# Optimization experiments

Measured on AMD Instinct MI355X. Metric: run time of the kernel, lower is better.

The kernel has to match this reference:

```python
import jax, jax.numpy as jnp
import numpy as np

B, L, C = 4, 2048, 2048
NH, HD, K = 32, 64, 16  # num_heads, head_dim, inner chunk size
LR = 1.0
EPS = 1e-6


def ln_fwd(x, w, b):
    # F.layer_norm over last dim (biased variance), eps=1e-6
    mu = x.mean(-1, keepdims=True)
    var = x.var(-1, keepdims=True)
    xhat = (x - mu) * jax.lax.rsqrt(var + EPS)
    return w * xhat + b


def ln_fused_l2_bwd(x, target, w, b):
    # grad wrt x of 0.5*||LN(x;w,b) - target||^2 fused with LN fwd
    D = x.shape[-1]
    mu = x.mean(-1, keepdims=True)
    var = x.var(-1, keepdims=True)
    std = jnp.sqrt(var + EPS)
    xhat = (x - mu) / std
    y = w * xhat + b
    g = (y - target) * w  # dL/d(xhat)
    return (D * g - g.sum(-1, keepdims=True) - xhat * (g * xhat).sum(-1, keepdims=True)) / (D * std)


def _inner_scan(XC, XB, XA, coeff, W1, b1, lnw, lnb):
    # per (batch, head): XC/XB/XA [n_chunk,K,HD], coeff [n_chunk,K,1], W1 [HD,HD], b1 [1,HD], lnw/lnb [HD]
    mask = jnp.tril(jnp.ones((K, K), XC.dtype))

    def step(carry, inp):
        W1c, b1c = carry
        xc, xb, xa, co = inp
        Z1 = xb @ W1c + b1c                       # [K,HD]
        grad = ln_fused_l2_bwd(Z1, xa - xb, lnw, lnb)
        Attn1 = mask * (xc @ xb.T)                # [K,K] causal
        b1_bar = b1c - (co * mask) @ grad         # [K,HD]
        Z1_bar = xc @ W1c - (co * Attn1) @ grad + b1_bar
        W1n = W1c - (co[-1] * xb).T @ grad        # fast-weight update with last coeff
        b1n = b1_bar[-1:]
        out = xc + ln_fwd(Z1_bar, lnw, lnb)       # post-LN residual
        return (W1n, b1n), out

    _, ys = jax.lax.scan(step, (W1, b1), (XC, XB, XA, coeff))
    return ys.reshape(-1, HD)  # [L,HD]


def setup_inputs() -> dict:
    key = jax.random.key(0)
    ks = jax.random.split(key, 9)
    s = 0.02
    return {
        'hidden_states': jax.random.normal(ks[0], (B, L, C), jnp.float32),
        'Wq': jax.random.normal(ks[1], (C, NH * HD), jnp.float32) * s,
        'Wk': jax.random.normal(ks[2], (C, NH * HD), jnp.float32) * s,
        'Wv': jax.random.normal(ks[3], (C, NH * HD), jnp.float32) * s,
        'Wo': jax.random.normal(ks[4], (NH * HD, C), jnp.float32) * s,
        'ilr_w': jax.random.normal(ks[5], (C, NH), jnp.float32) * s,
        'ilr_b': jnp.zeros((NH,), jnp.float32),
        'ln_weight': jnp.ones((NH, HD), jnp.float32),
        'ln_bias': jnp.zeros((NH, HD), jnp.float32),
        'W1': jax.random.normal(ks[6], (NH, HD, HD), jnp.float32) * s,
        'b1': jnp.zeros((NH, 1, HD), jnp.float32),
    }


def reference(hidden_states, Wq, Wk, Wv, Wo, ilr_w, ilr_b, ln_weight, ln_bias, W1, b1):
    n_chunk = L // K

    def split(x):  # [B,L,NH*HD] -> [B,NH,n_chunk,K,HD]
        return x.reshape(B, n_chunk, K, NH, HD).transpose(0, 3, 1, 2, 4)

    XC = split(hidden_states @ Wq)
    XB = split(hidden_states @ Wk)
    XA = split(hidden_states @ Wv)

    # sigmoid-gated per-token learning rates
    ilr = jax.nn.sigmoid(hidden_states @ ilr_w + ilr_b)          # [B,L,NH]
    ilr = ilr.reshape(B, n_chunk, K, NH).transpose(0, 3, 1, 2)[..., None]  # [B,NH,n_chunk,K,1]
    token_idx = 1.0 / jnp.arange(1, K + 1, dtype=jnp.float32)
    coeff = (LR * token_idx).reshape(1, 1, 1, K, 1) * ilr / HD

    per_head = jax.vmap(_inner_scan, in_axes=(0, 0, 0, 0, 0, 0, 0, 0))
    per_batch = jax.vmap(per_head, in_axes=(0, 0, 0, 0, None, None, None, None))
    XCW = per_batch(XC, XB, XA, coeff, W1, b1, ln_weight, ln_bias)  # [B,NH,L,HD]
    XCW = XCW.transpose(0, 2, 1, 3).reshape(B, L, NH * HD)
    return XCW @ Wo
```

## Files before the change

### kernel.cpp

```cpp
#include <hip/hip_runtime.h>
#include <hip/hip_bf16.h>

typedef __attribute__((ext_vector_type(8))) short bf16x8;
typedef __attribute__((ext_vector_type(4))) short bf16x4;
typedef __attribute__((ext_vector_type(4))) float f32x4;
typedef __attribute__((ext_vector_type(8))) unsigned short u16x8;
typedef unsigned short u16;

#define AS1(p) ((__attribute__((address_space(1))) void*)(p))
#define AS3(p) ((__attribute__((address_space(3))) void*)(p))
#define GLL16(g, l) __builtin_amdgcn_global_load_lds(AS1(g), AS3(l), 16, 0, 0)

__device__ __forceinline__ u16 f2bf(float x) {
  return __builtin_bit_cast(u16, __float2bfloat16(x));
}
__device__ __forceinline__ float bf2f(u16 u) {
  return __builtin_bit_cast(float, ((unsigned)u) << 16);
}
__device__ __forceinline__ f32x4 mfma16(bf16x8 a, bf16x8 b, f32x4 c) {
  return __builtin_amdgcn_mfma_f32_16x16x32_bf16(a, b, c, 0, 0, 0);
}
__device__ __forceinline__ f32x4 mfma16k(bf16x4 a, bf16x4 b, f32x4 c) {
#if defined(__HIP_DEVICE_COMPILE__)
#if __has_builtin(__builtin_amdgcn_mfma_f32_16x16x16bf16_1k)
  return __builtin_amdgcn_mfma_f32_16x16x16bf16_1k(a, b, c, 0, 0, 0);
#else
  f32x4 d;
  asm volatile("v_mfma_f32_16x16x16_bf16 %0, %1, %2, %3"
               : "=v"(d)
               : "v"(a), "v"(b), "v"(c));
  return d;
#endif
#else
  (void)a; (void)b;
  return c;
#endif
}
#define DPPADD(x, ctrl)                                                            \
  ((x) + __builtin_bit_cast(float, __builtin_amdgcn_update_dpp(                    \
             0, __builtin_bit_cast(int, (x)), (ctrl), 0xf, 0xf, true)))
__device__ __forceinline__ float rsum16(float x) {
  x = DPPADD(x, 0x128);
  x = DPPADD(x, 0x124);
  x = DPPADD(x, 0x122);
  x = DPPADD(x, 0x121);
  return x;
}

__global__ __launch_bounds__(256) void conv_bf16(const float* __restrict__ in,
                                                 u16* __restrict__ out) {
  size_t g = (size_t)blockIdx.x * 256 + threadIdx.x;
  const float4* p = reinterpret_cast<const float4*>(in) + g * 2;
  float4 a = p[0], b = p[1];
  u16x8 r;
  r[0] = f2bf(a.x); r[1] = f2bf(a.y); r[2] = f2bf(a.z); r[3] = f2bf(a.w);
  r[4] = f2bf(b.x); r[5] = f2bf(b.y); r[6] = f2bf(b.z); r[7] = f2bf(b.w);
  *reinterpret_cast<u16x8*>(out + g * 8) = r;
}

__global__ __launch_bounds__(256) void wt_conv(const float* __restrict__ W,
                                               u16* __restrict__ Wt, int Kd, int N) {
  __shared__ float t[64][65];
  const int n0 = blockIdx.x * 64, k0 = blockIdx.y * 64;
  const int tx = threadIdx.x & 63, ty = threadIdx.x >> 6;
#pragma unroll
  for (int rr = 0; rr < 16; ++rr) {
    int r = rr * 4 + ty;
    t[r][tx] = W[(size_t)(k0 + r) * N + n0 + tx];
  }
  __syncthreads();
#pragma unroll
  for (int rr = 0; rr < 16; ++rr) {
    int r = rr * 4 + ty;
    Wt[(size_t)(n0 + r) * Kd + k0 + tx] = f2bf(t[tx][r]);
  }
}

__global__ __launch_bounds__(256) void ilr_strip(const float* __restrict__ ilr_w,
                                                 u16* __restrict__ WcatT) {
  int g = blockIdx.x * 256 + threadIdx.x;
  int p = g >> 11, k = g & 2047;
  float v = (p < 32) ? ilr_w[k * 32 + p] : 0.f;
  WcatT[(size_t)(6144 + p) * 2048 + k] = f2bf(v);
}

template <int MODE>
__global__ __launch_bounds__(512) void gemm8p(const u16* __restrict__ A,
                                              const u16* __restrict__ Bt, int M, int N, int Kd,
                                              u16* __restrict__ O0, u16* __restrict__ O1,
                                              u16* __restrict__ O2,
                                              float* __restrict__ coeffOut,
                                              const float* __restrict__ ilrb,
                                              float* __restrict__ Cout) {
  __shared__ __align__(16) u16 Asm[2][2][8192];
  __shared__ __align__(16) u16 Bsm[2][2][8192];
  const int tid = threadIdx.x;
  const int lane = tid & 63, wid = tid >> 6;
  const int wr = wid >> 2, wc = wid & 3;
  const int l15 = lane & 15, l4 = lane >> 4;
  const int wc1 = wc & 1, wch = wc >> 1;
  const int swzm = (l15 & 3) ^ (((l15 >> 2) & 1) << 2);
  const int mT = blockIdx.y << 8, nT = blockIdx.x << 8;
  const int nKt = Kd >> 6;

#define STG_A(kt_, h_)                                                              \
  do {                                                                              \
    if ((kt_) < nKt) {                                                              \
      _Pragma("unroll") for (int i_ = 0; i_ < 2; ++i_) {                            \
        const int s_ = tid + 512 * i_;                                              \
        const int r_ = s_ >> 3;                                                     \
        const int sc_ = (s_ & 7) ^ (r_ & 3) ^ (((r_ >> 2) & 1) << 2);               \
        GLL16(A + (size_t)(mT + (h_) * 128 + r_) * Kd + (kt_) * 64 + sc_ * 8,       \
              &Asm[(kt_) & 1][h_][0] + s_ * 8);                                     \
      }                                                                             \
    }                                                                               \
  } while (0)
#define STG_B(kt_, h_)                                                              \
  do {                                                                              \
    if ((kt_) < nKt) {                                                              \
      _Pragma("unroll") for (int i_ = 0; i_ < 2; ++i_) {                            \
        const int s_ = tid + 512 * i_;                                              \
        const int r_ = s_ >> 3;                                                     \
        const int sc_ = (s_ & 7) ^ (r_ & 3) ^ (((r_ >> 2) & 1) << 2);               \
        const int rg_ = nT + (h_) * 128 + r_;                                       \
        if (rg_ < N)                                                                \
          GLL16(Bt + (size_t)rg_ * Kd + (kt_) * 64 + sc_ * 8,                       \
                &Bsm[(kt_) & 1][h_][0] + s_ * 8);                                   \
      }                                                                             \
    }                                                                               \
  } while (0)
#define RD_A(buf_, mi_, ks_)                                                        \
  (*(const bf16x8*)((const char*)&Asm[buf_][wr][0] + 128 * ((mi_) * 16 + l15) +     \
                    16 * ((l4 + 4 * (ks_)) ^ swzm)))
#define RD_B(buf_, ni_, ks_)                                                        \
  (*(const bf16x8*)((const char*)&Bsm[buf_][wch][0] +                               \
                    128 * (wc1 * 64 + (ni_) * 16 + l15) +                           \
                    16 * ((l4 + 4 * (ks_)) ^ swzm)))
#define BARRIER __builtin_amdgcn_s_barrier()
#define LGKM0                                                                       \
  do {                                                                              \
    asm volatile("s_waitcnt lgkmcnt(0)" ::: "memory");                              \
    __builtin_amdgcn_sched_barrier(0);                                              \
  } while (0)
#define VM4 asm volatile("s_waitcnt vmcnt(4)" ::: "memory")
#define PRIO1 __builtin_amdgcn_s_setprio(1)
#define PRIO0 __builtin_amdgcn_s_setprio(0)
#define QUAD(mh_, nh_)                                                              \
  _Pragma("unroll") for (int m4_ = 0; m4_ < 4; ++m4_)                               \
  _Pragma("unroll") for (int n2_ = 0; n2_ < 2; ++n2_)                               \
  _Pragma("unroll") for (int ks_ = 0; ks_ < 2; ++ks_)                               \
      acc[(mh_) * 4 + m4_][(nh_) * 2 + n2_] =                                       \
          mfma16(Af[(mh_) * 4 + m4_][ks_], Bf[(nh_) * 2 + n2_][ks_],                \
                 acc[(mh_) * 4 + m4_][(nh_) * 2 + n2_])

  f32x4 acc[8][4];
#pragma unroll
  for (int m = 0; m < 8; ++m)
#pragma unroll
    for (int n = 0; n < 4; ++n) acc[m][n] = (f32x4){0.f, 0.f, 0.f, 0.f};
  bf16x8 Af[8][2], Bf[4][2];

  STG_A(0, 0); STG_A(0, 1); STG_B(0, 0); STG_B(0, 1); STG_A(1, 0); STG_A(1, 1);
  VM4;
  BARRIER;

#pragma unroll 1
  for (int it = 0; it < (nKt >> 1); ++it) {
    const int T = 2 * it;
#pragma unroll
    for (int mi = 0; mi < 4; ++mi)
#pragma unroll
      for (int ks = 0; ks < 2; ++ks) Af[mi][ks] = RD_A(0, mi, ks);
#pragma unroll
    for (int ni = 0; ni < 2; ++ni)
#pragma unroll
      for (int ks = 0; ks < 2; ++ks) Bf[ni][ks] = RD_B(0, ni, ks);
    STG_B(T + 1, 0);
    BARRIER; LGKM0; PRIO1; QUAD(0, 0); PRIO0;
    BARRIER;
#pragma unroll
    for (int mi = 4; mi < 8; ++mi)
#pragma unroll
      for (int ks = 0; ks < 2; ++ks) Af[mi][ks] = RD_A(0, mi, ks);
    STG_B(T + 1, 1);
    BARRIER; LGKM0; PRIO1; QUAD(1, 0); PRIO0;
    BARRIER;
#pragma unroll
    for (int ni = 2; ni < 4; ++ni)
#pragma unroll
      for (int ks = 0; ks < 2; ++ks) Bf[ni][ks] = RD_B(0, ni, ks);
    STG_A(T + 2, 0);
    BARRIER; LGKM0; PRIO1; QUAD(0, 1); PRIO0;
    BARRIER;
    STG_A(T + 2, 1);
    BARRIER; LGKM0; PRIO1; QUAD(1, 1); PRIO0;
    VM4;
    BARRIER;
#pragma unroll
    for (int mi = 0; mi < 4; ++mi)
#pragma unroll
      for (int ks = 0; ks < 2; ++ks) Af[mi][ks] = RD_A(1, mi, ks);
#pragma unroll
    for (int ni = 0; ni < 2; ++ni)
#pragma unroll
      for (int ks = 0; ks < 2; ++ks) Bf[ni][ks] = RD_B(1, ni, ks);
    STG_B(T + 2, 0);
    BARRIER; LGKM0; PRIO1; QUAD(0, 0); PRIO0;
    BARRIER;
#pragma unroll
    for (int mi = 4; mi < 8; ++mi)
#pragma unroll
      for (int ks = 0; ks < 2; ++ks) Af[mi][ks] = RD_A(1, mi, ks);
    STG_B(T + 2, 1);
    BARRIER; LGKM0; PRIO1; QUAD(1, 0); PRIO0;
    BARRIER;
#pragma unroll
    for (int ni = 2; ni < 4; ++ni)
#pragma unroll
      for (int ks = 0; ks < 2; ++ks) Bf[ni][ks] = RD_B(1, ni, ks);
    STG_A(T + 3, 0);
    BARRIER; LGKM0; PRIO1; QUAD(0, 1); PRIO0;
    BARRIER;
    STG_A(T + 3, 1);
    BARRIER; LGKM0; PRIO1; QUAD(1, 1); PRIO0;
    VM4;
    BARRIER;
  }

#pragma unroll
  for (int mi = 0; mi < 8; ++mi) {
#pragma unroll
    for (int ni = 0; ni < 4; ++ni) {
      const int col = nT + wc * 64 + ni * 16 + l15;
#pragma unroll
      for (int e = 0; e < 4; ++e) {
        const int row = mT + wr * 128 + mi * 16 + l4 * 4 + e;
        float v = acc[mi][ni][e];
        if constexpr (MODE == 1) {
          Cout[(size_t)row * N + col] = v;
        } else {
          const int bb = row >> 11, lt = row & 2047;
          if (col < 6144) {
            const int mat = col >> 11;
            u16* base = (mat == 0) ? O0 : ((mat == 1) ? O1 : O2);
            const int hh = (col >> 6) & 31, dd = col & 63;
            base[(((size_t)(bb * 32 + hh)) * 2048 + lt) * 64 + dd] = f2bf(v);
          } else {
            const int h3 = col - 6144;
            if (h3 < 32) {
              const float x = v + ilrb[h3];
              const float sig = 1.f / (1.f + expf(-x));
              const int tok = lt & 15;
              coeffOut[((size_t)(bb * 32 + h3)) * 2048 + lt] =
                  sig * (1.f / (64.f * (float)(tok + 1)));
            }
          }
        }
      }
    }
  }
  (void)M;
#undef STG_A
#undef STG_B
#undef RD_A
#undef RD_B
#undef QUAD
}

__global__ __launch_bounds__(64) void ttt_scan(
    const u16* __restrict__ XC, const u16* __restrict__ XB, const u16* __restrict__ XA,
    const float* __restrict__ coeff, const float* __restrict__ lnw_g,
    const float* __restrict__ lnb_g, const float* __restrict__ W1g,
    const float* __restrict__ b1g, u16* __restrict__ XCW) {
  const int bh = blockIdx.x;
  const int b = bh >> 5, h = bh & 31;
  const int lane = threadIdx.x & 63;
  const int l15 = lane & 15, l4 = lane >> 4;

  const u16* xbb = XB + (size_t)bh * 131072;
  const u16* xcb = XC + (size_t)bh * 131072;
  const u16* xab = XA + (size_t)bh * 131072;
  const float* cob = coeff + (size_t)bh * 2048;

  float lnw4[4], lnb4[4], b1m[4];
#pragma unroll
  for (int cb = 0; cb < 4; ++cb) {
    lnw4[cb] = lnw_g[h * 64 + cb * 16 + l15];
    lnb4[cb] = lnb_g[h * 64 + cb * 16 + l15];
    b1m[cb] = b1g[h * 64 + cb * 16 + l15];
  }
  f32x4 mW[4][4];
#pragma unroll
  for (int kb = 0; kb < 4; ++kb)
#pragma unroll
    for (int cb = 0; cb < 4; ++cb)
#pragma unroll
      for (int e = 0; e < 4; ++e)
        mW[kb][cb][e] = W1g[(size_t)h * 4096 + (kb * 16 + l4 * 4 + e) * 64 + cb * 16 + l15];

  uint2 nxbA[4], nxcA[4];
  float nco[4], nco15, ncoL;
  const int foA = l15 * 128 + l4 * 8;
#define PF(cc)                                                                       \
  do {                                                                               \
    const char* pb = (const char*)(xbb + (cc) * 1024);                               \
    const char* pc = (const char*)(xcb + (cc) * 1024);                               \
    _Pragma("unroll") for (int kb = 0; kb < 4; ++kb) {                               \
      nxbA[kb] = *(const uint2*)(pb + foA + kb * 32);                                \
      nxcA[kb] = *(const uint2*)(pc + foA + kb * 32);                                \
    }                                                                                \
    _Pragma("unroll") for (int e = 0; e < 4; ++e) nco[e] = cob[(cc) * 16 + l4 * 4 + e]; \
    nco15 = cob[(cc) * 16 + 15];                                                     \
    ncoL = cob[(cc) * 16 + l15];                                                     \
  } while (0)

  PF(0);

#pragma unroll 1
  for (int c = 0; c < 128; ++c) {
    bf16x4 xbA[4], xcA[4];
#pragma unroll
    for (int kb = 0; kb < 4; ++kb) {
      xbA[kb] = __builtin_bit_cast(bf16x4, nxbA[kb]);
      xcA[kb] = __builtin_bit_cast(bf16x4, nxcA[kb]);
    }
    float co_own[4];
#pragma unroll
    for (int e = 0; e < 4; ++e) co_own[e] = nco[e];
    const float co15 = nco15, coL = ncoL;

    u16 sxa[4][4], sxb[4][4], sxc[4][4];
    {
      const u16* xap_ = xab + c * 1024;
      const u16* xbp_ = xbb + c * 1024;
      const u16* xcp_ = xcb + c * 1024;
#pragma unroll
      for (int cb = 0; cb < 4; ++cb)
#pragma unroll
        for (int e = 0; e < 4; ++e) {
          const int idx = (l4 * 4 + e) * 64 + cb * 16 + l15;
          sxa[cb][e] = xap_[idx];
          sxb[cb][e] = xbp_[idx];
          sxc[cb][e] = xcp_[idx];
        }
    }
    PF((c < 127) ? (c + 1) : 127);

    f32x4 pT = {0.f, 0.f, 0.f, 0.f};
#pragma unroll
    for (int kb = 0; kb < 4; ++kb) pT = mfma16k(xbA[kb], xcA[kb], pT);
    bf16x4 pTf;
#pragma unroll
    for (int e = 0; e < 4; ++e) {
      const int r = l4 * 4 + e;
      pTf[e] = (short)f2bf((r <= l15) ? pT[e] * (-coL) : 0.f);
    }

    bf16x4 w1b[4][4];
#pragma unroll
    for (int kb = 0; kb < 4; ++kb)
#pragma unroll
      for (int cb = 0; cb < 4; ++cb)
#pragma unroll
        for (int e = 0; e < 4; ++e) w1b[kb][cb][e] = (short)f2bf(mW[kb][cb][e]);

    f32x4 z[4], o2[4];
#pragma unroll
    for (int cb = 0; cb < 4; ++cb) {
      f32x4 a = {b1m[cb], b1m[cb], b1m[cb], b1m[cb]};
#pragma unroll
      for (int kb = 0; kb < 4; ++kb) a = mfma16k(xbA[kb], w1b[kb][cb], a);
      z[cb] = a;
      f32x4 a2 = {0.f, 0.f, 0.f, 0.f};
#pragma unroll
      for (int kb = 0; kb < 4; ++kb) a2 = mfma16k(xcA[kb], w1b[kb][cb], a2);
      o2[cb] = a2;
    }

    float gr[4][4];
#pragma unroll
    for (int e = 0; e < 4; ++e) {
      float zz[4];
#pragma unroll
      for (int cb = 0; cb < 4; ++cb) zz[cb] = z[cb][e];
      float s1 = zz[0] + zz[1] + zz[2] + zz[3];
      float s2 = zz[0] * zz[0] + zz[1] * zz[1] + zz[2] * zz[2] + zz[3] * zz[3];
      s1 = rsum16(s1);
      s2 = rsum16(s2);
      const float mu = s1 * 0.015625f;
      const float var = fmaxf(s2 * 0.015625f - mu * mu, 0.f);
      const float rstd = rsqrtf(var + 1e-6f);
      float xh[4], gl[4];
#pragma unroll
      for (int cb = 0; cb < 4; ++cb) {
        xh[cb] = (zz[cb] - mu) * rstd;
        const float tgt = bf2f(sxa[cb][e]) - bf2f(sxb[cb][e]);
        gl[cb] = (fmaf(lnw4[cb], xh[cb], lnb4[cb]) - tgt) * lnw4[cb];
      }
      float gs = gl[0] + gl[1] + gl[2] + gl[3];
      float gx = gl[0] * xh[0] + gl[1] * xh[1] + gl[2] * xh[2] + gl[3] * xh[3];
      gs = rsum16(gs);
      gx = rsum16(gx);
#pragma unroll
      for (int cb = 0; cb < 4; ++cb)
        gr[cb][e] = (64.f * gl[cb] - gs - xh[cb] * gx) * (rstd * 0.015625f);
    }

    float gtot[4], lower[4];
#pragma unroll
    for (int cb = 0; cb < 4; ++cb) {
      const float T = gr[cb][0] + gr[cb][1] + gr[cb][2] + gr[cb][3];
      const float t1 = __shfl_xor(T, 16, 64);
      const float t2 = __shfl_xor(T, 32, 64);
      const float t3 = __shfl_xor(t1, 32, 64);
      gtot[cb] = T + t1 + t2 + t3;
      lower[cb] = ((l4 & 1) ? t1 : 0.f) + ((l4 & 2) ? (t2 + t3) : 0.f);
    }

    bf16x4 grB[4];
#pragma unroll
    for (int cb = 0; cb < 4; ++cb)
#pragma unroll
      for (int e = 0; e < 4; ++e) grB[cb][e] = (short)f2bf(gr[cb][e]);

#pragma unroll
    for (int cb = 0; cb < 4; ++cb) o2[cb] = mfma16k(pTf, grB[cb], o2[cb]);

    bf16x4 xbU[4];
#pragma unroll
    for (int kb = 0; kb < 4; ++kb)
#pragma unroll
      for (int e = 0; e < 4; ++e)
        xbU[kb][e] = (short)f2bf(bf2f(sxb[kb][e]) * (-co15));
#pragma unroll
    for (int kb = 0; kb < 4; ++kb)
#pragma unroll
      for (int cb = 0; cb < 4; ++cb) mW[kb][cb] = mfma16k(xbU[kb], grB[cb], mW[kb][cb]);

    float ov[4][4];
#pragma unroll
    for (int cb = 0; cb < 4; ++cb) {
      float pfx = lower[cb];
#pragma unroll
      for (int e = 0; e < 4; ++e) {
        pfx += gr[cb][e];
        ov[cb][e] = o2[cb][e] + fmaf(-co_own[e], pfx, b1m[cb]);
      }
    }
#pragma unroll
    for (int e = 0; e < 4; ++e) {
      float s1 = ov[0][e] + ov[1][e] + ov[2][e] + ov[3][e];
      float s2 = ov[0][e] * ov[0][e] + ov[1][e] * ov[1][e] + ov[2][e] * ov[2][e] +
                 ov[3][e] * ov[3][e];
      s1 = rsum16(s1);
      s2 = rsum16(s2);
      const float mu = s1 * 0.015625f;
      const float var = fmaxf(s2 * 0.015625f - mu * mu, 0.f);
      const float rstd = rsqrtf(var + 1e-6f);
      const size_t rowg = (size_t)(b * 2048 + c * 16 + l4 * 4 + e) * 2048 + h * 64;
#pragma unroll
      for (int cb = 0; cb < 4; ++cb) {
        const float y = bf2f(sxc[cb][e]) + fmaf(lnw4[cb], (ov[cb][e] - mu) * rstd, lnb4[cb]);
        XCW[rowg + cb * 16 + l15] = f2bf(y);
      }
    }

#pragma unroll
    for (int cb = 0; cb < 4; ++cb) b1m[cb] = fmaf(-co15, gtot[cb], b1m[cb]);
  }
#undef PF
}

extern "C" void kernel_launch(void* const* d_in, const int* in_sizes, int n_in, void* d_out,
                              int out_size, void* d_ws, size_t ws_size, hipStream_t stream) {
  const float* hs = (const float*)d_in[0];
  const float* Wq = (const float*)d_in[1];
  const float* Wk = (const float*)d_in[2];
  const float* Wv = (const float*)d_in[3];
  const float* Wo = (const float*)d_in[4];
  const float* ilr_w = (const float*)d_in[5];
  const float* ilr_b = (const float*)d_in[6];
  const float* lnw = (const float*)d_in[7];
  const float* lnb = (const float*)d_in[8];
  const float* W1 = (const float*)d_in[9];
  const float* b1 = (const float*)d_in[10];
  float* out = (float*)d_out;

  if (ws_size < 93847552u) return;
  char* ws = (char*)d_ws;
  u16* hsb = (u16*)(ws + 0);
  u16* WcatT = (u16*)(ws + 33554432);
  u16* XCbf = (u16*)(ws + 59244544);
  float* coeffb = (float*)(ws + 92798976);
  u16* XCW = hsb;
  u16* WoT = (u16*)(ws + 33554432);
  u16* XBbf = (u16*)d_out;
  u16* XAbf = (u16*)((char*)d_out + 33554432);

  conv_bf16<<<8192, 256, 0, stream>>>(hs, hsb);
  wt_conv<<<dim3(32, 32), 256, 0, stream>>>(Wq, WcatT, 2048, 2048);
  wt_conv<<<dim3(32, 32), 256, 0, stream>>>(Wk, WcatT + (size_t)2048 * 2048, 2048, 2048);
  wt_conv<<<dim3(32, 32), 256, 0, stream>>>(Wv, WcatT + (size_t)4096 * 2048, 2048, 2048);
  ilr_strip<<<1024, 256, 0, stream>>>(ilr_w, WcatT);

  gemm8p<0><<<dim3(25, 32), 512, 0, stream>>>(hsb, WcatT, 8192, 6272, 2048, XCbf, XBbf, XAbf,
                                              coeffb, ilr_b, nullptr);
  wt_conv<<<dim3(32, 32), 256, 0, stream>>>(Wo, WoT, 2048, 2048);
  ttt_scan<<<128, 64, 0, stream>>>(XCbf, XBbf, XAbf, coeffb, lnw, lnb, W1, b1, XCW);
  gemm8p<1><<<dim3(8, 32), 512, 0, stream>>>(XCW, WoT, 8192, 2048, 2048, nullptr, nullptr,
                                             nullptr, nullptr, nullptr, out);

  (void)in_sizes; (void)n_in; (void)out_size;
}
```

Before: 650.6 us.

## Interleave two independent batch-head scans per wavefront in ttt_scan

Each ttt_scan block now processes two (batch, head) sequences at once (q and q+64), which halves the grid to 64 single-wave blocks. The two independent dependency chains are interleaved so their MFMA, shuffle and load latencies can overlap inside one wave. The cost is roughly double the register footprint, since both fast-weight matrices and both prefetch sets stay live, with a risk of spills. It also uses only 64 of the GPU's compute units instead of 128, so per-sequence serial latency has to fall enough to make up for the lost parallelism.

```diff
diff --git a/kernel.cpp b/kernel.cpp
--- a/kernel.cpp
+++ b/kernel.cpp
@@ -267,206 +267,242 @@
 #undef QUAD
 }
 
-__global__ __launch_bounds__(64) void ttt_scan(
+__global__ __launch_bounds__(64, 1) void ttt_scan(
     const u16* __restrict__ XC, const u16* __restrict__ XB, const u16* __restrict__ XA,
     const float* __restrict__ coeff, const float* __restrict__ lnw_g,
     const float* __restrict__ lnb_g, const float* __restrict__ W1g,
     const float* __restrict__ b1g, u16* __restrict__ XCW) {
-  const int bh = blockIdx.x;
-  const int b = bh >> 5, h = bh & 31;
+  const int q = blockIdx.x;
+  const int h = q & 31;
   const int lane = threadIdx.x & 63;
   const int l15 = lane & 15, l4 = lane >> 4;
 
-  const u16* xbb = XB + (size_t)bh * 131072;
-  const u16* xcb = XC + (size_t)bh * 131072;
-  const u16* xab = XA + (size_t)bh * 131072;
-  const float* cob = coeff + (size_t)bh * 2048;
-
-  float lnw4[4], lnb4[4], b1m[4];
+  const u16 *xbb[2], *xcb[2], *xab[2];
+  const float* cob[2];
+  int bseq[2];
+#pragma unroll
+  for (int s = 0; s < 2; ++s) {
+    const int bh = q + s * 64;
+    bseq[s] = bh >> 5;
+    xbb[s] = XB + (size_t)bh * 131072;
+    xcb[s] = XC + (size_t)bh * 131072;
+    xab[s] = XA + (size_t)bh * 131072;
+    cob[s] = coeff + (size_t)bh * 2048;
+  }
+
+  float lnw4[4], lnb4[4];
 #pragma unroll
   for (int cb = 0; cb < 4; ++cb) {
     lnw4[cb] = lnw_g[h * 64 + cb * 16 + l15];
     lnb4[cb] = lnb_g[h * 64 + cb * 16 + l15];
-    b1m[cb] = b1g[h * 64 + cb * 16 + l15];
-  }
-  f32x4 mW[4][4];
-#pragma unroll
-  for (int kb = 0; kb < 4; ++kb)
-#pragma unroll
-    for (int cb = 0; cb < 4; ++cb)
-#pragma unroll
-      for (int e = 0; e < 4; ++e)
-        mW[kb][cb][e] = W1g[(size_t)h * 4096 + (kb * 16 + l4 * 4 + e) * 64 + cb * 16 + l15];
-
-  uint2 nxbA[4], nxcA[4];
-  float nco[4], nco15, ncoL;
+  }
+  float b1m[2][4];
+  f32x4 mW[2][4][4];
+#pragma unroll
+  for (int s = 0; s < 2; ++s) {
+#pragma unroll
+    for (int cb = 0; cb < 4; ++cb) b1m[s][cb] = b1g[h * 64 + cb * 16 + l15];
+#pragma unroll
+    for (int kb = 0; kb < 4; ++kb)
+#pragma unroll
+      for (int cb = 0; cb < 4; ++cb)
+#pragma unroll
+        for (int e = 0; e < 4; ++e)
+          mW[s][kb][cb][e] =
+              W1g[(size_t)h * 4096 + (kb * 16 + l4 * 4 + e) * 64 + cb * 16 + l15];
+  }
+
+  uint2 nxbA[2][4], nxcA[2][4];
+  float nco[2][4], nco15[2], ncoL[2];
   const int foA = l15 * 128 + l4 * 8;
-#define PF(cc)                                                                       \
+#define PF(s, cc)                                                                    \
   do {                                                                               \
-    const char* pb = (const char*)(xbb + (cc) * 1024);                               \
-    const char* pc = (const char*)(xcb + (cc) * 1024);                               \
+    const char* pb = (const char*)(xbb[s] + (cc) * 1024);                            \
+    const char* pc = (const char*)(xcb[s] + (cc) * 1024);                            \
     _Pragma("unroll") for (int kb = 0; kb < 4; ++kb) {                               \
-      nxbA[kb] = *(const uint2*)(pb + foA + kb * 32);                                \
-      nxcA[kb] = *(const uint2*)(pc + foA + kb * 32);                                \
+      nxbA[s][kb] = *(const uint2*)(pb + foA + kb * 32);                             \
+      nxcA[s][kb] = *(const uint2*)(pc + foA + kb * 32);                             \
     }                                                                                \
-    _Pragma("unroll") for (int e = 0; e < 4; ++e) nco[e] = cob[(cc) * 16 + l4 * 4 + e]; \
-    nco15 = cob[(cc) * 16 + 15];                                                     \
-    ncoL = cob[(cc) * 16 + l15];                                                     \
+    _Pragma("unroll") for (int e = 0; e < 4; ++e)                                    \
+        nco[s][e] = cob[s][(cc) * 16 + l4 * 4 + e];                                  \
+    nco15[s] = cob[s][(cc) * 16 + 15];                                               \
+    ncoL[s] = cob[s][(cc) * 16 + l15];                                               \
   } while (0)
 
-  PF(0);
+#pragma unroll
+  for (int s = 0; s < 2; ++s) PF(s, 0);
 
 #pragma unroll 1
   for (int c = 0; c < 128; ++c) {
-    bf16x4 xbA[4], xcA[4];
-#pragma unroll
-    for (int kb = 0; kb < 4; ++kb) {
-      xbA[kb] = __builtin_bit_cast(bf16x4, nxbA[kb]);
-      xcA[kb] = __builtin_bit_cast(bf16x4, nxcA[kb]);
-    }
-    float co_own[4];
-#pragma unroll
-    for (int e = 0; e < 4; ++e) co_own[e] = nco[e];
-    const float co15 = nco15, coL = ncoL;
-
-    u16 sxa[4][4], sxb[4][4], sxc[4][4];
-    {
-      const u16* xap_ = xab + c * 1024;
-      const u16* xbp_ = xbb + c * 1024;
-      const u16* xcp_ = xcb + c * 1024;
+    bf16x4 xbA[2][4], xcA[2][4];
+    float co_own[2][4], co15[2], coL[2];
+#pragma unroll
+    for (int s = 0; s < 2; ++s) {
+#pragma unroll
+      for (int kb = 0; kb < 4; ++kb) {
+        xbA[s][kb] = __builtin_bit_cast(bf16x4, nxbA[s][kb]);
+        xcA[s][kb] = __builtin_bit_cast(bf16x4, nxcA[s][kb]);
+      }
+#pragma unroll
+      for (int e = 0; e < 4; ++e) co_own[s][e] = nco[s][e];
+      co15[s] = nco15[s];
+      coL[s] = ncoL[s];
+    }
+
+    u16 sxa[2][4][4], sxb[2][4][4], sxc[2][4][4];
+#pragma unroll
+    for (int s = 0; s < 2; ++s) {
+      const u16* xap_ = xab[s] + c * 1024;
+      const u16* xbp_ = xbb[s] + c * 1024;
+      const u16* xcp_ = xcb[s] + c * 1024;
 #pragma unroll
       for (int cb = 0; cb < 4; ++cb)
 #pragma unroll
         for (int e = 0; e < 4; ++e) {
           const int idx = (l4 * 4 + e) * 64 + cb * 16 + l15;
-          sxa[cb][e] = xap_[idx];
-          sxb[cb][e] = xbp_[idx];
-          sxc[cb][e] = xcp_[idx];
+          sxa[s][cb][e] = xap_[idx];
+          sxb[s][cb][e] = xbp_[idx];
+          sxc[s][cb][e] = xcp_[idx];
         }
     }
-    PF((c < 127) ? (c + 1) : 127);
-
-    f32x4 pT = {0.f, 0.f, 0.f, 0.f};
-#pragma unroll
-    for (int kb = 0; kb < 4; ++kb) pT = mfma16k(xbA[kb], xcA[kb], pT);
-    bf16x4 pTf;
-#pragma unroll
-    for (int e = 0; e < 4; ++e) {
-      const int r = l4 * 4 + e;
-      pTf[e] = (short)f2bf((r <= l15) ? pT[e] * (-coL) : 0.f);
-    }
-
-    bf16x4 w1b[4][4];
-#pragma unroll
-    for (int kb = 0; kb < 4; ++kb)
+    {
+      const int cc = (c < 127) ? (c + 1) : 127;
+#pragma unroll
+      for (int s = 0; s < 2; ++s) PF(s, cc);
+    }
+
+    bf16x4 pTf[2];
+#pragma unroll
+    for (int s = 0; s < 2; ++s) {
+      f32x4 pT = {0.f, 0.f, 0.f, 0.f};
+#pragma unroll
+      for (int kb = 0; kb < 4; ++kb) pT = mfma16k(xbA[s][kb], xcA[s][kb], pT);
+#pragma unroll
+      for (int e = 0; e < 4; ++e) {
+        const int r = l4 * 4 + e;
+        pTf[s][e] = (short)f2bf((r <= l15) ? pT[e] * (-coL[s]) : 0.f);
+      }
+    }
+
+    f32x4 z[2][4], o2[2][4];
+#pragma unroll
+    for (int s = 0; s < 2; ++s) {
+#pragma unroll
+      for (int cb = 0; cb < 4; ++cb) {
+        bf16x4 wk[4];
+#pragma unroll
+        for (int kb = 0; kb < 4; ++kb)
+#pragma unroll
+          for (int e = 0; e < 4; ++e) wk[kb][e] = (short)f2bf(mW[s][kb][cb][e]);
+        f32x4 a = {b1m[s][cb], b1m[s][cb], b1m[s][cb], b1m[s][cb]};
+#pragma unroll
+        for (int kb = 0; kb < 4; ++kb) a = mfma16k(xbA[s][kb], wk[kb], a);
+        z[s][cb] = a;
+        f32x4 a2 = {0.f, 0.f, 0.f, 0.f};
+#pragma unroll
+        for (int kb = 0; kb < 4; ++kb) a2 = mfma16k(xcA[s][kb], wk[kb], a2);
+        o2[s][cb] = a2;
+      }
+    }
+
+    float gr[2][4][4];
+#pragma unroll
+    for (int s = 0; s < 2; ++s) {
+#pragma unroll
+      for (int e = 0; e < 4; ++e) {
+        float zz[4];
+#pragma unroll
+        for (int cb = 0; cb < 4; ++cb) zz[cb] = z[s][cb][e];
+        float s1 = zz[0] + zz[1] + zz[2] + zz[3];
+        float s2 = zz[0] * zz[0] + zz[1] * zz[1] + zz[2] * zz[2] + zz[3] * zz[3];
+        s1 = rsum16(s1);
+        s2 = rsum16(s2);
+        const float mu = s1 * 0.015625f;
+        const float var = fmaxf(s2 * 0.015625f - mu * mu, 0.f);
+        const float rstd = rsqrtf(var + 1e-6f);
+        float xh[4], gl[4];
+#pragma unroll
+        for (int cb = 0; cb < 4; ++cb) {
+          xh[cb] = (zz[cb] - mu) * rstd;
+          const float tgt = bf2f(sxa[s][cb][e]) - bf2f(sxb[s][cb][e]);
+          gl[cb] = (fmaf(lnw4[cb], xh[cb], lnb4[cb]) - tgt) * lnw4[cb];
+        }
+        float gs = gl[0] + gl[1] + gl[2] + gl[3];
+        float gx = gl[0] * xh[0] + gl[1] * xh[1] + gl[2] * xh[2] + gl[3] * xh[3];
+        gs = rsum16(gs);
+        gx = rsum16(gx);
+#pragma unroll
+        for (int cb = 0; cb < 4; ++cb)
+          gr[s][cb][e] = (64.f * gl[cb] - gs - xh[cb] * gx) * (rstd * 0.015625f);
+      }
+    }
+
+#pragma unroll
+    for (int s = 0; s < 2; ++s) {
+      float gtot[4], lower[4];
+#pragma unroll
+      for (int cb = 0; cb < 4; ++cb) {
+        const float T = gr[s][cb][0] + gr[s][cb][1] + gr[s][cb][2] + gr[s][cb][3];
+        const float t1 = __shfl_xor(T, 16, 64);
+        const float t2 = __shfl_xor(T, 32, 64);
+        const float t3 = __shfl_xor(t1, 32, 64);
+        gtot[cb] = T + t1 + t2 + t3;
+        lower[cb] = ((l4 & 1) ? t1 : 0.f) + ((l4 & 2) ? (t2 + t3) : 0.f);
+      }
+
+      bf16x4 grB[4];
 #pragma unroll
       for (int cb = 0; cb < 4; ++cb)
 #pragma unroll
-        for (int e = 0; e < 4; ++e) w1b[kb][cb][e] = (short)f2bf(mW[kb][cb][e]);
-
-    f32x4 z[4], o2[4];
-#pragma unroll
-    for (int cb = 0; cb < 4; ++cb) {
-      f32x4 a = {b1m[cb], b1m[cb], b1m[cb], b1m[cb]};
-#pragma unroll
-      for (int kb = 0; kb < 4; ++kb) a = mfma16k(xbA[kb], w1b[kb][cb], a);
-      z[cb] = a;
-      f32x4 a2 = {0.f, 0.f, 0.f, 0.f};
-#pragma unroll
-      for (int kb = 0; kb < 4; ++kb) a2 = mfma16k(xcA[kb], w1b[kb][cb], a2);
-      o2[cb] = a2;
-    }
-
-    float gr[4][4];
-#pragma unroll
-    for (int e = 0; e < 4; ++e) {
-      float zz[4];
-#pragma unroll
-      for (int cb = 0; cb < 4; ++cb) zz[cb] = z[cb][e];
-      float s1 = zz[0] + zz[1] + zz[2] + zz[3];
-      float s2 = zz[0] * zz[0] + zz[1] * zz[1] + zz[2] * zz[2] + zz[3] * zz[3];
-      s1 = rsum16(s1);
-      s2 = rsum16(s2);
-      const float mu = s1 * 0.015625f;
-      const float var = fmaxf(s2 * 0.015625f - mu * mu, 0.f);
-      const float rstd = rsqrtf(var + 1e-6f);
-      float xh[4], gl[4];
+        for (int e = 0; e < 4; ++e) grB[cb][e] = (short)f2bf(gr[s][cb][e]);
+
+#pragma unroll
+      for (int cb = 0; cb < 4; ++cb) o2[s][cb] = mfma16k(pTf[s], grB[cb], o2[s][cb]);
+
+      bf16x4 xbU[4];
+#pragma unroll
+      for (int kb = 0; kb < 4; ++kb)
+#pragma unroll
+        for (int e = 0; e < 4; ++e)
+          xbU[kb][e] = (short)f2bf(bf2f(sxb[s][kb][e]) * (-co15[s]));
+#pragma unroll
+      for (int kb = 0; kb < 4; ++kb)
+#pragma unroll
+        for (int cb = 0; cb < 4; ++cb)
+          mW[s][kb][cb] = mfma16k(xbU[kb], grB[cb], mW[s][kb][cb]);
+
+      float ov[4][4];
 #pragma unroll
       for (int cb = 0; cb < 4; ++cb) {
-        xh[cb] = (zz[cb] - mu) * rstd;
-        const float tgt = bf2f(sxa[cb][e]) - bf2f(sxb[cb][e]);
-        gl[cb] = (fmaf(lnw4[cb], xh[cb], lnb4[cb]) - tgt) * lnw4[cb];
-      }
-      float gs = gl[0] + gl[1] + gl[2] + gl[3];
-      float gx = gl[0] * xh[0] + gl[1] * xh[1] + gl[2] * xh[2] + gl[3] * xh[3];
-      gs = rsum16(gs);
-      gx = rsum16(gx);
-#pragma unroll
-      for (int cb = 0; cb < 4; ++cb)
-        gr[cb][e] = (64.f * gl[cb] - gs - xh[cb] * gx) * (rstd * 0.015625f);
-    }
-
-    float gtot[4], lower[4];
-#pragma unroll
-    for (int cb = 0; cb < 4; ++cb) {
-      const float T = gr[cb][0] + gr[cb][1] + gr[cb][2] + gr[cb][3];
-      const float t1 = __shfl_xor(T, 16, 64);
-      const float t2 = __shfl_xor(T, 32, 64);
-      const float t3 = __shfl_xor(t1, 32, 64);
-      gtot[cb] = T + t1 + t2 + t3;
-      lower[cb] = ((l4 & 1) ? t1 : 0.f) + ((l4 & 2) ? (t2 + t3) : 0.f);
-    }
-
-    bf16x4 grB[4];
-#pragma unroll
-    for (int cb = 0; cb < 4; ++cb)
-#pragma unroll
-      for (int e = 0; e < 4; ++e) grB[cb][e] = (short)f2bf(gr[cb][e]);
-
-#pragma unroll
-    for (int cb = 0; cb < 4; ++cb) o2[cb] = mfma16k(pTf, grB[cb], o2[cb]);
-
-    bf16x4 xbU[4];
-#pragma unroll
-    for (int kb = 0; kb < 4; ++kb)
-#pragma unroll
-      for (int e = 0; e < 4; ++e)
-        xbU[kb][e] = (short)f2bf(bf2f(sxb[kb][e]) * (-co15));
-#pragma unroll
-    for (int kb = 0; kb < 4; ++kb)
-#pragma unroll
-      for (int cb = 0; cb < 4; ++cb) mW[kb][cb] = mfma16k(xbU[kb], grB[cb], mW[kb][cb]);
-
-    float ov[4][4];
-#pragma unroll
-    for (int cb = 0; cb < 4; ++cb) {
-      float pfx = lower[cb];
+        float pfx = lower[cb];
+#pragma unroll
+        for (int e = 0; e < 4; ++e) {
+          pfx += gr[s][cb][e];
+          ov[cb][e] = o2[s][cb][e] + fmaf(-co_own[s][e], pfx, b1m[s][cb]);
+        }
+      }
 #pragma unroll
       for (int e = 0; e < 4; ++e) {
-        pfx += gr[cb][e];
-        ov[cb][e] = o2[cb][e] + fmaf(-co_own[e], pfx, b1m[cb]);
-      }
-    }
-#pragma unroll
-    for (int e = 0; e < 4; ++e) {
-      float s1 = ov[0][e] + ov[1][e] + ov[2][e] + ov[3][e];
-      float s2 = ov[0][e] * ov[0][e] + ov[1][e] * ov[1][e] + ov[2][e] * ov[2][e] +
-                 ov[3][e] * ov[3][e];
-      s1 = rsum16(s1);
-      s2 = rsum16(s2);
-      const float mu = s1 * 0.015625f;
-      const float var = fmaxf(s2 * 0.015625f - mu * mu, 0.f);
-      const float rstd = rsqrtf(var + 1e-6f);
-      const size_t rowg = (size_t)(b * 2048 + c * 16 + l4 * 4 + e) * 2048 + h * 64;
-#pragma unroll
-      for (int cb = 0; cb < 4; ++cb) {
-        const float y = bf2f(sxc[cb][e]) + fmaf(lnw4[cb], (ov[cb][e] - mu) * rstd, lnb4[cb]);
-        XCW[rowg + cb * 16 + l15] = f2bf(y);
-      }
-    }
-
-#pragma unroll
-    for (int cb = 0; cb < 4; ++cb) b1m[cb] = fmaf(-co15, gtot[cb], b1m[cb]);
+        float s1 = ov[0][e] + ov[1][e] + ov[2][e] + ov[3][e];
+        float s2 = ov[0][e] * ov[0][e] + ov[1][e] * ov[1][e] + ov[2][e] * ov[2][e] +
+                   ov[3][e] * ov[3][e];
+        s1 = rsum16(s1);
+        s2 = rsum16(s2);
+        const float mu = s1 * 0.015625f;
+        const float var = fmaxf(s2 * 0.015625f - mu * mu, 0.f);
+        const float rstd = rsqrtf(var + 1e-6f);
+        const size_t rowg = (size_t)(bseq[s] * 2048 + c * 16 + l4 * 4 + e) * 2048 + h * 64;
+#pragma unroll
+        for (int cb = 0; cb < 4; ++cb) {
+          const float y =
+              bf2f(sxc[s][cb][e]) + fmaf(lnw4[cb], (ov[cb][e] - mu) * rstd, lnb4[cb]);
+          XCW[rowg + cb * 16 + l15] = f2bf(y);
+        }
+      }
+
+#pragma unroll
+      for (int cb = 0; cb < 4; ++cb) b1m[s][cb] = fmaf(-co15[s], gtot[cb], b1m[s][cb]);
+    }
   }
 #undef PF
 }
@@ -506,7 +542,7 @@
   gemm8p<0><<<dim3(25, 32), 512, 0, stream>>>(hsb, WcatT, 8192, 6272, 2048, XCbf, XBbf, XAbf,
                                               coeffb, ilr_b, nullptr);
   wt_conv<<<dim3(32, 32), 256, 0, stream>>>(Wo, WoT, 2048, 2048);
-  ttt_scan<<<128, 64, 0, stream>>>(XCbf, XBbf, XAbf, coeffb, lnw, lnb, W1, b1, XCW);
+  ttt_scan<<<64, 64, 0, stream>>>(XCbf, XBbf, XAbf, coeffb, lnw, lnb, W1, b1, XCW);
   gemm8p<1><<<dim3(8, 32), 512, 0, stream>>>(XCW, WoT, 8192, 2048, 2048, nullptr, nullptr,
                                              nullptr, nullptr, nullptr, out);
 
```

Measured after the change: 992.2 us. +52.5%, slower.
